# Optimization experiments

Measured on AMD Instinct MI355X. Metric: run time of the kernel, lower is better.

The kernel has to match this reference:

```python
import jax, jax.numpy as jnp
import numpy as np

# Config mirroring TransFusionHead / HungarianAssigner3D defaults (nuScenes)
PC_RANGE = (-54.0, -54.0, -5.0, 54.0, 54.0, 3.0)
CLS_W, CLS_ALPHA, CLS_GAMMA = 0.15, 0.25, 2.0
REG_W, IOU_W = 0.25, 0.25
EPS = 1e-12

B, N, M, C = 8, 4096, 1024, 10


def setup_inputs() -> dict:
    key = jax.random.key(0)
    k1, k2, k3, k4 = jax.random.split(key, 4)

    def make_boxes(k, n):
        ka, kb, kc, kd = jax.random.split(k, 4)
        xy = jax.random.uniform(ka, (B, n, 2), minval=-54.0, maxval=54.0)
        z = jax.random.uniform(kb, (B, n, 1), minval=-5.0, maxval=3.0)
        dims = jax.random.uniform(kc, (B, n, 3), minval=0.5, maxval=6.0)
        yaw = jax.random.uniform(kd, (B, n, 1), minval=-np.pi, maxval=np.pi)
        return jnp.concatenate([xy, z, dims, yaw], axis=-1).astype(jnp.float32)

    bboxes = make_boxes(k1, N)          # [B, N, 7]
    gt_bboxes = make_boxes(k2, M)       # [B, M, 7]
    cls_pred = jax.random.normal(k3, (B, N, C), dtype=jnp.float32)  # logits
    gt_labels = jax.random.randint(k4, (B, M), 0, C).astype(jnp.int32)
    return {"bboxes": bboxes, "gt_bboxes": gt_bboxes,
            "cls_pred": cls_pred, "gt_labels": gt_labels}


def _bev_iou(a, b):
    # a: [B,N,7], b: [B,M,7] -> axis-aligned BEV IoU [B,N,M]
    xa1 = a[..., 0] - a[..., 3] * 0.5; ya1 = a[..., 1] - a[..., 4] * 0.5
    xa2 = a[..., 0] + a[..., 3] * 0.5; ya2 = a[..., 1] + a[..., 4] * 0.5
    xb1 = b[..., 0] - b[..., 3] * 0.5; yb1 = b[..., 1] - b[..., 4] * 0.5
    xb2 = b[..., 0] + b[..., 3] * 0.5; yb2 = b[..., 1] + b[..., 4] * 0.5
    ix1 = jnp.maximum(xa1[:, :, None], xb1[:, None, :])
    iy1 = jnp.maximum(ya1[:, :, None], yb1[:, None, :])
    ix2 = jnp.minimum(xa2[:, :, None], xb2[:, None, :])
    iy2 = jnp.minimum(ya2[:, :, None], yb2[:, None, :])
    inter = jnp.clip(ix2 - ix1, 0) * jnp.clip(iy2 - iy1, 0)
    area_a = jnp.clip(xa2 - xa1, 0) * jnp.clip(ya2 - ya1, 0)
    area_b = jnp.clip(xb2 - xb1, 0) * jnp.clip(yb2 - yb1, 0)
    union = area_a[:, :, None] + area_b[:, None, :] - inter
    return inter / jnp.clip(union, 1e-6)


def reference(bboxes, gt_bboxes, cls_pred, gt_labels):
    # --- focal classification cost ---
    p = jax.nn.sigmoid(cls_pred)                                   # [B,N,C]
    neg = -jnp.log(1.0 - p + EPS) * (1.0 - CLS_ALPHA) * p ** CLS_GAMMA
    pos = -jnp.log(p + EPS) * CLS_ALPHA * (1.0 - p) ** CLS_GAMMA
    diff = (pos - neg) * CLS_W                                     # [B,N,C]
    idx = jnp.broadcast_to(gt_labels[:, None, :], (diff.shape[0], diff.shape[1], gt_labels.shape[1]))
    cls_cost = jnp.take_along_axis(diff, idx, axis=2)              # [B,N,M]

    pc_start = jnp.asarray(PC_RANGE[0:2], dtype=bboxes.dtype)
    pc_rng = jnp.asarray(PC_RANGE[3:5], dtype=bboxes.dtype) - pc_start
    a_xy = (bboxes[..., :2] - pc_start) / pc_rng                   # [B,N,2]
    b_xy = (gt_bboxes[..., :2] - pc_start) / pc_rng                # [B,M,2]
    reg_cost = jnp.abs(a_xy[:, :, None, :] - b_xy[:, None, :, :]).sum(-1) * REG_W

    # --- IoU cost (axis-aligned BEV IoU, CPU path of lidar_box_iou3d) ---
    iou = _bev_iou(bboxes, gt_bboxes)                              # [B,N,M]

    cost = cls_cost + reg_cost - iou * IOU_W
    return cost
```

## Files before the change

### kernel.cpp

```cpp
#include <hip/hip_runtime.h>
#include <hip/hip_bf16.h>

#define BB 8
#define NN 4096
#define MM 1024
#define CC 10

#define ROWS_PER_BLOCK 32
#define BLOCKS_PER_BATCH (NN / ROWS_PER_BLOCK)

__device__ __forceinline__ float fast_rcp(float x) {
    float r;
    asm("v_rcp_f32 %0, %1" : "=v"(r) : "v"(x));
    return r;
}

__global__ __launch_bounds__(256, 4)
void transfusion_cost_kernel(const float* __restrict__ bboxes,
                             const float* __restrict__ gt_bboxes,
                             const float* __restrict__ cls_pred,
                             const int*   __restrict__ gt_labels,
                             float* __restrict__ out)
{
    const int tid  = threadIdx.x;
    const int lane = tid & 63;
    const int wave = tid >> 6;

    const int b  = blockIdx.x / BLOCKS_PER_BATCH;
    const int n0 = (blockIdx.x % BLOCKS_PER_BATCH) * ROWS_PER_BLOCK;

    const float SCL = 0.25f / 108.0f;

    const int m0 = wave * 256 + 4 * lane;
    const float* gtb = gt_bboxes + ((size_t)b * MM + m0) * 7;
    const int*   gtl = gt_labels + (size_t)b * MM + m0;

    float gx1[4], gy1[4], gx2[4], gy2[4], areaB[4], bxs[4], bys[4];
    int   lbl[4];
#pragma unroll
    for (int j = 0; j < 4; ++j) {
        const float* g = gtb + j * 7;
        const float x  = g[0];
        const float y  = g[1];
        const float dx = g[3];
        const float dy = g[4];
        const float x1 = x - 0.5f * dx, x2 = x + 0.5f * dx;
        const float y1 = y - 0.5f * dy, y2 = y + 0.5f * dy;
        gx1[j] = x1; gy1[j] = y1; gx2[j] = x2; gy2[j] = y2;
        areaB[j] = fmaxf(x2 - x1, 0.0f) * fmaxf(y2 - y1, 0.0f);
        bxs[j] = (x + 54.0f) * SCL;
        bys[j] = (y + 54.0f) * SCL;
        lbl[j] = gtl[j];
    }

    const int c = (lane < CC) ? lane : 0;
    const float* arow = bboxes   + ((size_t)b * NN + n0) * 7;
    const float* crow = cls_pred + ((size_t)b * NN + n0) * CC;
    float*       orow = out + ((size_t)b * NN + n0) * MM + m0;

#pragma unroll 2
    for (int r = 0; r < ROWS_PER_BLOCK; ++r) {
        const float* a = arow + r * 7;
        const float ax  = a[0];
        const float ay  = a[1];
        const float adx = a[3];
        const float ady = a[4];
        const float logit = crow[r * CC + c];

        const float xa1 = ax - 0.5f * adx, xa2 = ax + 0.5f * adx;
        const float ya1 = ay - 0.5f * ady, ya2 = ay + 0.5f * ady;
        const float areaA = fmaxf(xa2 - xa1, 0.0f) * fmaxf(ya2 - ya1, 0.0f);
        const float axs = (ax + 54.0f) * SCL;
        const float ays = (ay + 54.0f) * SCL;

        const float p   = 1.0f / (1.0f + expf(-logit));
        const float omp = 1.0f - p;
        const float pos = -logf(p   + 1e-12f) * 0.25f * omp * omp;
        const float neg = -logf(omp + 1e-12f) * 0.75f * p * p;
        const float dval = (pos - neg) * 0.15f;

        float vv[4];
#pragma unroll
        for (int j = 0; j < 4; ++j) {
            const float ix1 = fmaxf(xa1, gx1[j]);
            const float iy1 = fmaxf(ya1, gy1[j]);
            const float ix2 = fminf(xa2, gx2[j]);
            const float iy2 = fminf(ya2, gy2[j]);
            const float iw  = fmaxf(ix2 - ix1, 0.0f);
            const float ih  = fmaxf(iy2 - iy1, 0.0f);
            const float inter = iw * ih;
            const float uni   = areaA + areaB[j] - inter;
            const float iou   = inter * fast_rcp(fmaxf(uni, 1e-6f));

            const float cls = __shfl(dval, lbl[j], 64);
            const float reg = fabsf(axs - bxs[j]) + fabsf(ays - bys[j]);

            vv[j] = cls + reg - 0.25f * iou;
        }

        *reinterpret_cast<float4*>(orow + (size_t)r * MM) =
            make_float4(vv[0], vv[1], vv[2], vv[3]);
    }
}

extern "C" void kernel_launch(void* const* d_in, const int* in_sizes, int n_in,
                              void* d_out, int out_size, void* d_ws, size_t ws_size,
                              hipStream_t stream) {
    const float* bboxes    = (const float*)d_in[0];
    const float* gt_bboxes = (const float*)d_in[1];
    const float* cls_pred  = (const float*)d_in[2];
    const int*   gt_labels = (const int*)d_in[3];
    float* out = (float*)d_out;

    const int grid = BB * BLOCKS_PER_BATCH;
    transfusion_cost_kernel<<<grid, 256, 0, stream>>>(bboxes, gt_bboxes, cls_pred,
                                                      gt_labels, out);
}
```

Before: 170.3 us.

## Precompute focal class cost in separate kernel and halve rows per block

Moves the sigmoid/log focal-cost computation into a separate pre-pass kernel that writes a [B,N,C] table to workspace. The main kernel then loads the precomputed value instead of recomputing the transcendentals in every block. The main kernel also uses 16 rows per block instead of 32, asks for 8 blocks per CU in its launch bounds instead of 4, unrolls the row loop 4 times, and replaces __shfl with a direct ds_bpermute using pre-shifted labels. The extra kernel launch and workspace round-trip add overhead, and the new path depends on enough workspace being available.

```diff
diff --git a/kernel.cpp b/kernel.cpp
--- a/kernel.cpp
+++ b/kernel.cpp
@@ -1,12 +1,13 @@
 #include <hip/hip_runtime.h>
 #include <hip/hip_bf16.h>
+
 
 #define BB 8
 #define NN 4096
 #define MM 1024
 #define CC 10
 
-#define ROWS_PER_BLOCK 32
+#define ROWS_PER_BLOCK 16
 #define BLOCKS_PER_BATCH (NN / ROWS_PER_BLOCK)
 
 __device__ __forceinline__ float fast_rcp(float x) {
@@ -15,11 +16,27 @@
     return r;
 }
 
-__global__ __launch_bounds__(256, 4)
+__device__ __forceinline__ float focal_diff(float logit) {
+    const float p   = 1.0f / (1.0f + expf(-logit));
+    const float omp = 1.0f - p;
+    const float pos = -logf(p   + 1e-12f) * 0.25f * omp * omp;
+    const float neg = -logf(omp + 1e-12f) * 0.75f * p * p;
+    return (pos - neg) * 0.15f;
+}
+
+__global__ __launch_bounds__(256)
+void focal_diff_kernel(const float* __restrict__ cls_pred, float* __restrict__ diff) {
+    const int i = blockIdx.x * 256 + threadIdx.x;
+    diff[i] = focal_diff(cls_pred[i]);
+}
+
+template <bool USE_WS>
+__global__ __launch_bounds__(256, 8)
 void transfusion_cost_kernel(const float* __restrict__ bboxes,
                              const float* __restrict__ gt_bboxes,
                              const float* __restrict__ cls_pred,
                              const int*   __restrict__ gt_labels,
+                             const float* __restrict__ diff,
                              float* __restrict__ out)
 {
     const int tid  = threadIdx.x;
@@ -36,7 +53,7 @@
     const int*   gtl = gt_labels + (size_t)b * MM + m0;
 
     float gx1[4], gy1[4], gx2[4], gy2[4], areaB[4], bxs[4], bys[4];
-    int   lbl[4];
+    int   lbl4[4];
 #pragma unroll
     for (int j = 0; j < 4; ++j) {
         const float* g = gtb + j * 7;
@@ -50,22 +67,29 @@
         areaB[j] = fmaxf(x2 - x1, 0.0f) * fmaxf(y2 - y1, 0.0f);
         bxs[j] = (x + 54.0f) * SCL;
         bys[j] = (y + 54.0f) * SCL;
-        lbl[j] = gtl[j];
+        lbl4[j] = gtl[j] << 2;
     }
 
     const int c = (lane < CC) ? lane : 0;
     const float* arow = bboxes   + ((size_t)b * NN + n0) * 7;
     const float* crow = cls_pred + ((size_t)b * NN + n0) * CC;
+    const float* drow = USE_WS ? diff + ((size_t)b * NN + n0) * CC : nullptr;
     float*       orow = out + ((size_t)b * NN + n0) * MM + m0;
 
-#pragma unroll 2
+#pragma unroll 4
     for (int r = 0; r < ROWS_PER_BLOCK; ++r) {
         const float* a = arow + r * 7;
         const float ax  = a[0];
         const float ay  = a[1];
         const float adx = a[3];
         const float ady = a[4];
-        const float logit = crow[r * CC + c];
+
+        float dval;
+        if (USE_WS) {
+            dval = drow[r * CC + c];
+        } else {
+            dval = focal_diff(crow[r * CC + c]);
+        }
 
         const float xa1 = ax - 0.5f * adx, xa2 = ax + 0.5f * adx;
         const float ya1 = ay - 0.5f * ady, ya2 = ay + 0.5f * ady;
@@ -73,11 +97,7 @@
         const float axs = (ax + 54.0f) * SCL;
         const float ays = (ay + 54.0f) * SCL;
 
-        const float p   = 1.0f / (1.0f + expf(-logit));
-        const float omp = 1.0f - p;
-        const float pos = -logf(p   + 1e-12f) * 0.25f * omp * omp;
-        const float neg = -logf(omp + 1e-12f) * 0.75f * p * p;
-        const float dval = (pos - neg) * 0.15f;
+        const int dbits = __float_as_int(dval);
 
         float vv[4];
 #pragma unroll
@@ -92,7 +112,7 @@
             const float uni   = areaA + areaB[j] - inter;
             const float iou   = inter * fast_rcp(fmaxf(uni, 1e-6f));
 
-            const float cls = __shfl(dval, lbl[j], 64);
+            const float cls = __int_as_float(__builtin_amdgcn_ds_bpermute(lbl4[j], dbits));
             const float reg = fabsf(axs - bxs[j]) + fabsf(ays - bys[j]);
 
             vv[j] = cls + reg - 0.25f * iou;
@@ -113,6 +133,15 @@
     float* out = (float*)d_out;
 
     const int grid = BB * BLOCKS_PER_BATCH;
-    transfusion_cost_kernel<<<grid, 256, 0, stream>>>(bboxes, gt_bboxes, cls_pred,
-                                                      gt_labels, out);
+    const size_t diff_bytes = (size_t)BB * NN * CC * sizeof(float);
+
+    if (ws_size >= diff_bytes) {
+        float* diff = (float*)d_ws;
+        focal_diff_kernel<<<(BB * NN * CC) / 256, 256, 0, stream>>>(cls_pred, diff);
+        transfusion_cost_kernel<true><<<grid, 256, 0, stream>>>(
+            bboxes, gt_bboxes, cls_pred, gt_labels, diff, out);
+    } else {
+        transfusion_cost_kernel<false><<<grid, 256, 0, stream>>>(
+            bboxes, gt_bboxes, cls_pred, gt_labels, nullptr, out);
+    }
 }
```

New measurement: 161.1 us. -5.4%, faster.
